# Kernel tuning notes

Hardware: AMD Instinct MI355X
Metric: run time of the kernel (lower is better)

The kernel has to match this reference:

```python
import jax, jax.numpy as jnp
import numpy as np

B, S, DIM = 2, 2048, 2048
QH, KVH = 32, 8
HD = DIM // QH            # 64
KV_DIM = HD * KVH         # 512
MAX_LEN = 2048
SCALE = HD ** -0.5
NEG_INF = -1e30


def _rope_cache(seq_len, head_dim, max_len, theta=10000.0, factor=8.0):
    # faithful to generate_sin_cos_pos_emb (causal branch, offset=0),
    # cache built at max_len then sliced to seq_len by the caller
    idx = np.arange(0, head_dim, 2, dtype=np.float64) / head_dim
    inv_freq = 1.0 / theta ** idx
    if factor > 1.0:
        seq_eff = max(max_len, max_len)  # generate called with seq_len=max_length
        adj = (factor * seq_eff / max_len - (factor - 1.0)) ** (head_dim / (head_dim - 2.0))
        inv_freq = 1.0 / (theta * adj) ** idx
    pos = np.arange(0, max_len, dtype=np.float64)
    freqs = np.einsum('i,j->ij', pos, inv_freq)
    emb = np.concatenate([freqs, freqs], axis=-1)  # [max_len, head_dim]
    cos = jnp.asarray(np.cos(emb)[:seq_len], dtype=jnp.float32)
    sin = jnp.asarray(np.sin(emb)[:seq_len], dtype=jnp.float32)
    return cos, sin


def _rotate_half(x):
    x1, x2 = jnp.split(x, 2, axis=-1)
    return jnp.concatenate([-x2, x1], axis=-1)


def _apply_rope(x, cos, sin):
    # x: [B, H, S, D]; cos/sin: [S, D]
    return x * cos + _rotate_half(x) * sin


def setup_inputs() -> dict:
    key = jax.random.key(0)
    ks = jax.random.split(key, 11)
    s = 0.02
    return {
        'query': jax.random.normal(ks[0], (B, S, DIM), jnp.float32),
        'key':   jax.random.normal(ks[1], (B, S, DIM), jnp.float32),
        'value': jax.random.normal(ks[2], (B, S, DIM), jnp.float32),
        'w_q': jax.random.normal(ks[3], (DIM, DIM), jnp.float32) * s,
        'b_q': jnp.zeros((DIM,), jnp.float32),
        'w_k': jax.random.normal(ks[4], (DIM, KV_DIM), jnp.float32) * s,
        'b_k': jnp.zeros((KV_DIM,), jnp.float32),
        'w_v': jax.random.normal(ks[5], (DIM, KV_DIM), jnp.float32) * s,
        'b_v': jnp.zeros((KV_DIM,), jnp.float32),
        'w_o': jax.random.normal(ks[6], (DIM, DIM), jnp.float32) * s,
        'b_o': jnp.zeros((DIM,), jnp.float32),
    }


def reference(query, key, value, w_q, b_q, w_k, b_k, w_v, b_v, w_o, b_o):
    # projections (weights stored as [in, out])
    q = query @ w_q + b_q                                    # [B,S,DIM]
    k = key   @ w_k + b_k                                    # [B,S,KV_DIM]
    v = value @ w_v + b_v                                    # [B,S,KV_DIM]

    q = q.reshape(B, S, QH, HD).transpose(0, 2, 1, 3)        # [B,QH,S,HD]
    k = k.reshape(B, S, KVH, HD).transpose(0, 2, 1, 3)       # [B,KVH,S,HD]
    v = v.reshape(B, S, KVH, HD).transpose(0, 2, 1, 3)       # [B,KVH,S,HD]

    cos, sin = _rope_cache(S, HD, MAX_LEN)
    q = _apply_rope(q, cos, sin)
    k = _apply_rope(k, cos, sin)

    # GQA: group queries per kv head (equivalent to repeat_interleave on K/V)
    G = QH // KVH
    qg = q.reshape(B, KVH, G, S, HD)
    scores = jnp.einsum('bhgqd,bhkd->bhgqk', qg, k) * SCALE  # [B,KVH,G,S,S]
    causal = jnp.tril(jnp.ones((S, S), dtype=bool))
    scores = jnp.where(causal, scores, NEG_INF)
    probs = jax.nn.softmax(scores, axis=-1)
    ctx = jnp.einsum('bhgqk,bhkd->bhgqd', probs, v)          # [B,KVH,G,S,HD]
    ctx = ctx.reshape(B, QH, S, HD).transpose(0, 2, 1, 3).reshape(B, S, DIM)
    return ctx @ w_o + b_o                                   # [B,S,DIM]
```

## Files before the change

kernel.cpp:

```cpp
#include <hip/hip_runtime.h>
#include <hip/hip_bf16.h>

typedef __hip_bfloat16 bf16_t;
typedef __attribute__((ext_vector_type(8))) short bf16x8;
typedef __attribute__((ext_vector_type(4))) float f32x4;

#define S_LEN   2048
#define D_MODEL 2048
#define N_QH    32
#define N_KVH   8
#define HEAD_D  64
#define KV_D    512
#define M_ROWS  4096
#define QK_SCALE (0.125f * 1.44269504088896340736f)
#define NQT     16

__global__ void wt_conv_all_kernel(const float* __restrict__ wq, const float* __restrict__ wk,
                                   const float* __restrict__ wv, const float* __restrict__ wo,
                                   bf16_t* __restrict__ tq, bf16_t* __restrict__ tk,
                                   bf16_t* __restrict__ tv, bf16_t* __restrict__ to,
                                   float* __restrict__ cosT, float* __restrict__ sinT) {
    const int x = blockIdx.x;
    if (x == 160) {
        int j = threadIdx.x & 31;
        double invf = pow(10000.0, -(double)(2 * j) / 64.0);
#pragma unroll
        for (int i = 0; i < 4; i++) {
            int pos = blockIdx.y * 32 + i * 8 + (threadIdx.x >> 5);
            double a = (double)pos * invf;
            cosT[pos * 32 + j] = (float)cos(a);
            sinT[pos * 32 + j] = (float)sin(a);
        }
        return;
    }
    __shared__ float tile[32][33];
    const float* W; bf16_t* Wt; int N, nb;
    if (x < 64)       { W = wq; Wt = tq; N = D_MODEL; nb = x; }
    else if (x < 80)  { W = wk; Wt = tk; N = KV_D;    nb = x - 64; }
    else if (x < 96)  { W = wv; Wt = tv; N = KV_D;    nb = x - 80; }
    else              { W = wo; Wt = to; N = D_MODEL; nb = x - 96; }
    const int K = D_MODEL;
    int n0 = nb * 32, k0 = blockIdx.y * 32;
    int tx = threadIdx.x & 31, ty = threadIdx.x >> 5;
#pragma unroll
    for (int i = 0; i < 4; i++) {
        int r = ty + i * 8;
        tile[r][tx] = W[(size_t)(k0 + r) * N + n0 + tx];
    }
    __syncthreads();
#pragma unroll
    for (int i = 0; i < 4; i++) {
        int r = ty + i * 8;
        Wt[(size_t)(n0 + r) * K + k0 + tx] = __float2bfloat16(tile[tx][r]);
    }
}

struct __align__(8) bf16x4s { bf16_t x, y, z, w; };

__device__ __forceinline__ void async_copy16(const bf16_t* g, bf16_t* l) {
    __builtin_amdgcn_global_load_lds((const __attribute__((address_space(1))) void*)g,
                                     (__attribute__((address_space(3))) void*)l, 16, 0, 0);
}

template <int ROPE, int OUTF32, int QSCALE>
__global__ __launch_bounds__(256, 2)
void gqa_gemm_kernel(const bf16_t* __restrict__ A, const bf16_t* __restrict__ Bt,
                     const float* __restrict__ bias, void* __restrict__ Cout,
                     int M, int N, int K,
                     const float* __restrict__ cosT, const float* __restrict__ sinT) {
    __shared__ __align__(16) bf16_t As[128 * 64];
    __shared__ __align__(16) bf16_t Bs[128 * 64];

    const int t = threadIdx.x;
    const int bx = blockIdx.x;
    const int xcd = bx & 7, j = bx >> 3;
    const int am0 = (((xcd >> 1) << 3) + (j >> 3)) * 128;
    const int bn0 = (((xcd & 1) << 3) + (j & 7)) * 128;

    const int l = t & 63, w = t >> 6;
    const int wr = w >> 1, wc = w & 1;
    const int lr = l & 15, lk = l >> 4;

    f32x4 acc[4][4];
#pragma unroll
    for (int i = 0; i < 4; i++)
#pragma unroll
        for (int jx = 0; jx < 4; jx++) acc[i][jx] = (f32x4)0.0f;

    const int r0 = t >> 3;
    const int c  = (t & 7) ^ (r0 & 7);
    const bf16_t* aptr = A + (size_t)(am0 + r0) * K + c * 8;
    const bf16_t* bptr = Bt + (size_t)(bn0 + r0) * K + c * 8;
    bf16_t* aLds = As + r0 * 64 + (t & 7) * 8;
    bf16_t* bLds = Bs + r0 * 64 + (t & 7) * 8;

    for (int k0 = 0; k0 < K; k0 += 64) {
#pragma unroll
        for (int s = 0; s < 4; ++s) {
            async_copy16(aptr + (size_t)(s * 32) * K + k0, aLds + s * 2048);
            async_copy16(bptr + (size_t)(s * 32) * K + k0, bLds + s * 2048);
        }
        __syncthreads();

        bf16x8 af[4][2], bfr[4][2];
#pragma unroll
        for (int mi = 0; mi < 4; mi++)
#pragma unroll
            for (int ks = 0; ks < 2; ks++)
                af[mi][ks] = *(const bf16x8*)&As[(wr * 64 + mi * 16 + lr) * 64 +
                                 ((ks * 32 + lk * 8) ^ ((lr & 7) << 3))];
#pragma unroll
        for (int ni = 0; ni < 4; ni++)
#pragma unroll
            for (int ks = 0; ks < 2; ks++)
                bfr[ni][ks] = *(const bf16x8*)&Bs[(wc * 64 + ni * 16 + lr) * 64 +
                                  ((ks * 32 + lk * 8) ^ ((lr & 7) << 3))];
#pragma unroll
        for (int mi = 0; mi < 4; mi++)
#pragma unroll
            for (int ni = 0; ni < 4; ni++)
#pragma unroll
                for (int ks = 0; ks < 2; ks++)
                    acc[mi][ni] = __builtin_amdgcn_mfma_f32_16x16x32_bf16(
                        af[mi][ks], bfr[ni][ks], acc[mi][ni], 0, 0, 0);
        __syncthreads();
    }

#pragma unroll
    for (int mi = 0; mi < 4; mi++) {
#pragma unroll
        for (int reg = 0; reg < 4; reg++) {
            int row = am0 + wr * 64 + mi * 16 + lk * 4 + reg;
            if (OUTF32) {
                float* out = (float*)Cout;
#pragma unroll
                for (int ni = 0; ni < 4; ni++) {
                    int col = bn0 + wc * 64 + ni * 16 + lr;
                    out[(size_t)row * N + col] = acc[mi][ni][reg] + bias[col];
                }
            } else if (ROPE) {
                bf16_t* out = (bf16_t*)Cout;
                int pos = row & (S_LEN - 1);
#pragma unroll
                for (int np = 0; np < 2; np++) {
                    int jj = np * 16 + lr;
                    float cs = cosT[pos * 32 + jj];
                    float sn = sinT[pos * 32 + jj];
                    int col1 = bn0 + wc * 64 + np * 16 + lr;
                    float x1 = acc[mi][np][reg] + bias[col1];
                    float x2 = acc[mi][np + 2][reg] + bias[col1 + 32];
                    float o1 = x1 * cs - x2 * sn;
                    float o2 = x2 * cs + x1 * sn;
                    if (QSCALE) { o1 *= QK_SCALE; o2 *= QK_SCALE; }
                    out[(size_t)row * N + col1]      = __float2bfloat16(o1);
                    out[(size_t)row * N + col1 + 32] = __float2bfloat16(o2);
                }
            } else {
                bf16_t* out = (bf16_t*)Cout;
#pragma unroll
                for (int ni = 0; ni < 4; ni++) {
                    int col = bn0 + wc * 64 + ni * 16 + lr;
                    out[(size_t)row * N + col] =
                        __float2bfloat16(acc[mi][ni][reg] + bias[col]);
                }
            }
        }
    }
}

__global__ __launch_bounds__(256, 4)
void gqa_kvc_kernel(const float* __restrict__ Key, const float* __restrict__ Val,
                    const float* __restrict__ Query,
                    const bf16_t* __restrict__ Wtk, const bf16_t* __restrict__ Wtv,
                    const float* __restrict__ bk, const float* __restrict__ bv,
                    bf16_t* __restrict__ Kout, bf16_t* __restrict__ VtOut,
                    bf16_t* __restrict__ Qbf,
                    const float* __restrict__ cosT, const float* __restrict__ sinT) {
    __shared__ __align__(16) char smem[9216];
    bf16_t* As  = (bf16_t*)smem;
    bf16_t* Bs  = (bf16_t*)(smem + 4096);
    bf16_t* VtE = (bf16_t*)smem;

    const int bx = blockIdx.x;
    const int t = threadIdx.x;

    if (bx >= 1024) {
        int tid = (bx - 1024) * 256 + t;
        const int total = M_ROWS * D_MODEL / 4;
#pragma unroll 4
        for (int i = tid; i < total; i += 512 * 256) {
            float4 v = ((const float4*)Query)[i];
            bf16x4s o;
            o.x = __float2bfloat16(v.x);
            o.y = __float2bfloat16(v.y);
            o.z = __float2bfloat16(v.z);
            o.w = __float2bfloat16(v.w);
            ((bf16x4s*)Qbf)[i] = o;
        }
        return;
    }

    constexpr int K = D_MODEL;
    const int xcd = bx & 7;
    const int j   = bx >> 3;
    const int z   = xcd >> 2;
    const int am0 = (((xcd & 3) << 4) + (j >> 3)) * 64;
    const int bn0 = (j & 7) * 64;

    const float* A32  = z ? Val : Key;
    const bf16_t* Bt  = z ? Wtv : Wtk;
    const float* bias = z ? bv : bk;

    const int l = t & 63, w = t >> 6;
    const int lr = l & 15, lk = l >> 4;

    f32x4 acc[4];
#pragma unroll
    for (int jx = 0; jx < 4; jx++) acc[jx] = (f32x4)0.0f;

    const int sr = t >> 2;
    const int sc = (t & 3) * 8;
    const float*  aptr = A32 + (size_t)(am0 + sr) * K + sc;
    const bf16_t* bptr = Bt + (size_t)(bn0 + sr) * K + sc;
    bf16_t* aLds = As + sr * 32 + sc;
    bf16_t* bLds = Bs + t * 8;

    float4 pa0 = ((const float4*)aptr)[0];
    float4 pa1 = ((const float4*)aptr)[1];

    for (int it = 0; it < K / 32; ++it) {
        union { bf16x8 v; bf16_t e[8]; } u;
        u.e[0] = __float2bfloat16(pa0.x); u.e[1] = __float2bfloat16(pa0.y);
        u.e[2] = __float2bfloat16(pa0.z); u.e[3] = __float2bfloat16(pa0.w);
        u.e[4] = __float2bfloat16(pa1.x); u.e[5] = __float2bfloat16(pa1.y);
        u.e[6] = __float2bfloat16(pa1.z); u.e[7] = __float2bfloat16(pa1.w);
        *(bf16x8*)aLds = u.v;
        async_copy16(bptr + it * 32, bLds);
        __builtin_amdgcn_sched_barrier(0);
        if (it + 1 < K / 32) {
            const float* ap = aptr + (it + 1) * 32;
            pa0 = ((const float4*)ap)[0];
            pa1 = ((const float4*)ap)[1];
            __builtin_amdgcn_sched_barrier(0);
            asm volatile("s_waitcnt lgkmcnt(0) vmcnt(2)" ::: "memory");
        } else {
            asm volatile("s_waitcnt lgkmcnt(0) vmcnt(0)" ::: "memory");
        }
        __builtin_amdgcn_sched_barrier(0);
        __builtin_amdgcn_s_barrier();
        __builtin_amdgcn_sched_barrier(0);

        bf16x8 af = *(const bf16x8*)&As[(w * 16 + lr) * 32 + lk * 8];
        bf16x8 bfr[4];
#pragma unroll
        for (int ni = 0; ni < 4; ni++)
            bfr[ni] = *(const bf16x8*)&Bs[(ni * 16 + lr) * 32 + lk * 8];
#pragma unroll
        for (int ni = 0; ni < 4; ni++)
            acc[ni] = __builtin_amdgcn_mfma_f32_16x16x32_bf16(af, bfr[ni], acc[ni], 0, 0, 0);
        __builtin_amdgcn_sched_barrier(0);
        __builtin_amdgcn_s_barrier();
        __builtin_amdgcn_sched_barrier(0);
    }

    if (z == 0) {
#pragma unroll
        for (int reg = 0; reg < 4; reg++) {
            int row = am0 + w * 16 + lk * 4 + reg;
            int pos = row & (S_LEN - 1);
#pragma unroll
            for (int np = 0; np < 2; np++) {
                int jj = np * 16 + lr;
                float cs = cosT[pos * 32 + jj];
                float sn = sinT[pos * 32 + jj];
                int col1 = bn0 + np * 16 + lr;
                float x1 = acc[np][reg] + bias[col1];
                float x2 = acc[np + 2][reg] + bias[col1 + 32];
                Kout[(size_t)row * KV_D + col1]      = __float2bfloat16(x1 * cs - x2 * sn);
                Kout[(size_t)row * KV_D + col1 + 32] = __float2bfloat16(x2 * cs + x1 * sn);
            }
        }
    } else {
        __syncthreads();
#pragma unroll
        for (int ni = 0; ni < 4; ni++) {
            bf16x4s pk;
            pk.x = __float2bfloat16(acc[ni][0] + bias[bn0 + ni * 16 + lr]);
            pk.y = __float2bfloat16(acc[ni][1] + bias[bn0 + ni * 16 + lr]);
            pk.z = __float2bfloat16(acc[ni][2] + bias[bn0 + ni * 16 + lr]);
            pk.w = __float2bfloat16(acc[ni][3] + bias[bn0 + ni * 16 + lr]);
            *(bf16x4s*)&VtE[(ni * 16 + lr) * 72 + w * 16 + lk * 4] = pk;
        }
        __syncthreads();
        const int d = t & 63, w2 = t >> 6;
        const int bI = am0 >> 11;
        const int kvhI = bn0 >> 6;
        const int sl = (am0 & (S_LEN - 1)) + w2 * 16;
        bf16_t* dst = VtOut + ((size_t)(bI * N_KVH + kvhI) * HEAD_D + d) * S_LEN + sl;
        const bf16_t* src = &VtE[d * 72 + w2 * 16];
        *(bf16x8*)dst       = *(const bf16x8*)src;
        *(bf16x8*)(dst + 8) = *(const bf16x8*)(src + 8);
    }
}

__device__ __forceinline__ void stage_K8(const bf16_t* KB, bf16_t* dst, int kt, int t) {
    const int skey = t >> 3;
    const int c    = (t & 7) ^ (skey & 7);
    async_copy16(KB + (size_t)(kt * 64 + skey) * KV_D + c * 8, dst + t * 8);
}
__device__ __forceinline__ void stage_V8(const bf16_t* VTb, bf16_t* dst, int kt, int t) {
    const int sd = t >> 3;
    const int c  = (t & 7) ^ (sd & 7);
    async_copy16(VTb + (size_t)sd * S_LEN + kt * 64 + c * 8, dst + t * 8);
}

__global__ __launch_bounds__(512, 4)
void gqa_attn_kernel(const bf16_t* __restrict__ Q, const bf16_t* __restrict__ Kb,
                     const bf16_t* __restrict__ VT, bf16_t* __restrict__ Ctx) {
    __shared__ __align__(16) bf16_t Ks[2][64 * 64];
    __shared__ __align__(16) bf16_t Vs[2][64 * 64];
    __shared__ __align__(16) bf16_t Pw[8][16 * 72];

    const int t = threadIdx.x, l = t & 63, w = t >> 6;
    const int lr = l & 15, lk = l >> 4;

    const int flat = blockIdx.x;
    const int xcd = flat & 7, j0 = flat >> 3;
    const int combo  = xcd * 2 + (j0 >> 5);
    const int within = j0 & 31;
    const int b   = combo >> 3;
    const int kvh = combo & 7;
    const int h   = kvh * 4 + (within >> 3);
    const int p   = within & 7;

    bf16x8 vones;
#pragma unroll
    for (int i = 0; i < 8; i++) vones[i] = (short)0x3F80;

    const bf16_t* KB  = Kb + (size_t)b * S_LEN * KV_D + kvh * HEAD_D;
    const bf16_t* VTb = VT + ((size_t)(b * N_KVH + kvh) * HEAD_D) * S_LEN;

#pragma unroll
    for (int half = 0; half < 2; ++half) {
        const int qt  = half ? (NQT - 1 - p) : p;
        const int q0w = qt * 128 + w * 16;
        const int qg  = q0w + lr;

        bf16x8 qf[2];
        {
            const bf16_t* qrow = Q + ((size_t)(b * S_LEN + qg)) * D_MODEL + h * HEAD_D;
            qf[0] = *(const bf16x8*)(qrow + lk * 8);
            qf[1] = *(const bf16x8*)(qrow + 32 + lk * 8);
        }

        f32x4 oaccT[4];
        f32x4 oaccS = (f32x4)0.0f;
#pragma unroll
        for (int df = 0; df < 4; df++) oaccT[df] = (f32x4)0.0f;

        const int nkt = 2 * qt + 2;

        stage_K8(KB, Ks[0], 0, t);
        stage_V8(VTb, Vs[0], 0, t);
        __syncthreads();

        int cur = 0;
        for (int kt = 0; kt < nkt; ++kt) {
            const bool pre = (kt + 1 < nkt);
            if (pre) {
                stage_K8(KB, Ks[cur ^ 1], kt + 1, t);
                stage_V8(VTb, Vs[cur ^ 1], kt + 1, t);
            }

            if (kt * 64 <= q0w + 15) {
                const bool diag = (kt * 64 + 63 > q0w);

                f32x4 sfrT[4];
#pragma unroll
                for (int ni = 0; ni < 4; ni++) sfrT[ni] = (f32x4)0.0f;
                __builtin_amdgcn_s_setprio(1);
#pragma unroll
                for (int ni = 0; ni < 4; ni++)
#pragma unroll
                    for (int ks = 0; ks < 2; ks++) {
                        bf16x8 kf = *(const bf16x8*)&Ks[cur][(ni * 16 + lr) * 64 +
                                        ((ks * 32 + lk * 8) ^ ((lr & 7) << 3))];
                        sfrT[ni] = __builtin_amdgcn_mfma_f32_16x16x32_bf16(kf, qf[ks],
                                                                           sfrT[ni], 0, 0, 0);
                    }
                __builtin_amdgcn_s_setprio(0);

#pragma unroll
                for (int ni = 0; ni < 4; ni++) {
                    float sc0 = sfrT[ni][0], sc1 = sfrT[ni][1];
                    float sc2 = sfrT[ni][2], sc3 = sfrT[ni][3];
                    if (diag) {
                        int kbase = kt * 64 + ni * 16 + lk * 4;
                        if (kbase + 0 > qg) sc0 = -1e30f;
                        if (kbase + 1 > qg) sc1 = -1e30f;
                        if (kbase + 2 > qg) sc2 = -1e30f;
                        if (kbase + 3 > qg) sc3 = -1e30f;
                    }
                    bf16x4s pk;
                    pk.x = __float2bfloat16(exp2f(sc0));
                    pk.y = __float2bfloat16(exp2f(sc1));
                    pk.z = __float2bfloat16(exp2f(sc2));
                    pk.w = __float2bfloat16(exp2f(sc3));
                    *(bf16x4s*)&Pw[w][lr * 72 + ni * 16 + lk * 4] = pk;
                }

                __builtin_amdgcn_s_setprio(1);
#pragma unroll
                for (int ks = 0; ks < 2; ks++) {
                    bf16x8 pf = *(const bf16x8*)&Pw[w][lr * 72 + ks * 32 + lk * 8];
                    oaccS = __builtin_amdgcn_mfma_f32_16x16x32_bf16(vones, pf, oaccS, 0, 0, 0);
#pragma unroll
                    for (int df = 0; df < 4; df++) {
                        bf16x8 vf = *(const bf16x8*)&Vs[cur][(df * 16 + lr) * 64 +
                                        ((ks * 32 + lk * 8) ^ ((lr & 7) << 3))];
                        oaccT[df] = __builtin_amdgcn_mfma_f32_16x16x32_bf16(vf, pf,
                                            oaccT[df], 0, 0, 0);
                    }
                }
                __builtin_amdgcn_s_setprio(0);
            }

            __syncthreads();
            cur ^= 1;
        }

        {
            float inv = 1.0f / oaccS[0];
            bf16_t* crow = Ctx + ((size_t)(b * S_LEN + qg)) * D_MODEL + h * HEAD_D;
#pragma unroll
            for (int df = 0; df < 4; df++) {
                bf16x4s ov;
                ov.x = __float2bfloat16(oaccT[df][0] * inv);
                ov.y = __float2bfloat16(oaccT[df][1] * inv);
                ov.z = __float2bfloat16(oaccT[df][2] * inv);
                ov.w = __float2bfloat16(oaccT[df][3] * inv);
                *(bf16x4s*)(crow + df * 16 + lk * 4) = ov;
            }
        }
    }
}

extern "C" void kernel_launch(void* const* d_in, const int* in_sizes, int n_in,
                              void* d_out, int out_size, void* d_ws, size_t ws_size,
                              hipStream_t stream) {
    const float* query = (const float*)d_in[0];
    const float* key_  = (const float*)d_in[1];
    const float* value = (const float*)d_in[2];
    const float* w_q = (const float*)d_in[3];
    const float* b_q = (const float*)d_in[4];
    const float* w_k = (const float*)d_in[5];
    const float* b_k = (const float*)d_in[6];
    const float* w_v = (const float*)d_in[7];
    const float* b_v = (const float*)d_in[8];
    const float* w_o = (const float*)d_in[9];
    const float* b_o = (const float*)d_in[10];
    float* out = (float*)d_out;

    char* ws = (char*)d_ws;
    bf16_t* Abuf = (bf16_t*)(ws);
    bf16_t* qb   = (bf16_t*)(ws + (size_t)(16 << 20));
    bf16_t* kb   = (bf16_t*)(ws + (size_t)(32 << 20));
    bf16_t* vt   = (bf16_t*)(ws + (size_t)(36 << 20));
    bf16_t* wtq  = (bf16_t*)(ws + (size_t)(40 << 20));
    bf16_t* wtk  = (bf16_t*)(ws + (size_t)(48 << 20));
    bf16_t* wtv  = (bf16_t*)(ws + (size_t)(50 << 20));
    bf16_t* wto  = (bf16_t*)(ws + (size_t)(52 << 20));
    float* cosT  = (float*)(ws + (size_t)(60 << 20));
    float* sinT  = (float*)(ws + (size_t)(60 << 20) + (256 << 10));

    wt_conv_all_kernel<<<dim3(161, 64), 256, 0, stream>>>(w_q, w_k, w_v, w_o,
                                                          wtq, wtk, wtv, wto, cosT, sinT);

    gqa_kvc_kernel<<<1536, 256, 0, stream>>>(key_, value, query, wtk, wtv,
                                             b_k, b_v, kb, vt, Abuf, cosT, sinT);

    gqa_gemm_kernel<1, 0, 1><<<512, 256, 0, stream>>>(
        Abuf, wtq, b_q, qb, M_ROWS, D_MODEL, D_MODEL, cosT, sinT);

    gqa_attn_kernel<<<512, 512, 0, stream>>>(qb, kb, vt, Abuf);

    gqa_gemm_kernel<0, 1, 0><<<512, 256, 0, stream>>>(
        Abuf, wto, b_o, out, M_ROWS, D_MODEL, D_MODEL, cosT, sinT);
}
```

Baseline: 211.2 us.

## Fuse Q/K/V projections into one GEMM launch after a single bf16 prep pass

```diff
diff --git a/kernel.cpp b/kernel.cpp
--- a/kernel.cpp
+++ b/kernel.cpp
@@ -15,47 +15,70 @@
 #define QK_SCALE (0.125f * 1.44269504088896340736f)
 #define NQT     16
 
-__global__ void wt_conv_all_kernel(const float* __restrict__ wq, const float* __restrict__ wk,
-                                   const float* __restrict__ wv, const float* __restrict__ wo,
-                                   bf16_t* __restrict__ tq, bf16_t* __restrict__ tk,
-                                   bf16_t* __restrict__ tv, bf16_t* __restrict__ to,
-                                   float* __restrict__ cosT, float* __restrict__ sinT) {
-    const int x = blockIdx.x;
-    if (x == 160) {
-        int j = threadIdx.x & 31;
+struct __align__(8) bf16x4s { bf16_t x, y, z, w; };
+
+__global__ void prep_kernel(const float* __restrict__ wq, const float* __restrict__ wk,
+                            const float* __restrict__ wv, const float* __restrict__ wo,
+                            bf16_t* __restrict__ tq, bf16_t* __restrict__ tk,
+                            bf16_t* __restrict__ tv, bf16_t* __restrict__ to,
+                            const float* __restrict__ query, const float* __restrict__ key_,
+                            const float* __restrict__ value,
+                            bf16_t* __restrict__ qbf, bf16_t* __restrict__ kbf,
+                            bf16_t* __restrict__ vbf,
+                            float* __restrict__ cosT, float* __restrict__ sinT) {
+    const int bx = blockIdx.x, t = threadIdx.x;
+    if (bx < 10240) {
+        __shared__ float tile[32][33];
+        const float* W; bf16_t* Wt; int N, nb, kt;
+        if (bx < 4096)      { W = wq; Wt = tq; N = D_MODEL; nb = bx & 63;          kt = bx >> 6; }
+        else if (bx < 5120) { int i = bx - 4096; W = wk; Wt = tk; N = KV_D; nb = i & 15; kt = i >> 4; }
+        else if (bx < 6144) { int i = bx - 5120; W = wv; Wt = tv; N = KV_D; nb = i & 15; kt = i >> 4; }
+        else                { int i = bx - 6144; W = wo; Wt = to; N = D_MODEL; nb = i & 63; kt = i >> 6; }
+        const int K = D_MODEL;
+        int n0 = nb * 32, k0 = kt * 32;
+        int tx = t & 31, ty = t >> 5;
+#pragma unroll
+        for (int i = 0; i < 4; i++) {
+            int r = ty + i * 8;
+            tile[r][tx] = W[(size_t)(k0 + r) * N + n0 + tx];
+        }
+        __syncthreads();
+#pragma unroll
+        for (int i = 0; i < 4; i++) {
+            int r = ty + i * 8;
+            Wt[(size_t)(n0 + r) * K + k0 + tx] = __float2bfloat16(tile[tx][r]);
+        }
+        return;
+    }
+    if (bx < 10304) {
+        int blk = bx - 10240;
+        int j = t & 31;
         double invf = pow(10000.0, -(double)(2 * j) / 64.0);
 #pragma unroll
         for (int i = 0; i < 4; i++) {
-            int pos = blockIdx.y * 32 + i * 8 + (threadIdx.x >> 5);
+            int pos = blk * 32 + i * 8 + (t >> 5);
             double a = (double)pos * invf;
             cosT[pos * 32 + j] = (float)cos(a);
             sinT[pos * 32 + j] = (float)sin(a);
         }
         return;
     }
-    __shared__ float tile[32][33];
-    const float* W; bf16_t* Wt; int N, nb;
-    if (x < 64)       { W = wq; Wt = tq; N = D_MODEL; nb = x; }
-    else if (x < 80)  { W = wk; Wt = tk; N = KV_D;    nb = x - 64; }
-    else if (x < 96)  { W = wv; Wt = tv; N = KV_D;    nb = x - 80; }
-    else              { W = wo; Wt = to; N = D_MODEL; nb = x - 96; }
-    const int K = D_MODEL;
-    int n0 = nb * 32, k0 = blockIdx.y * 32;
-    int tx = threadIdx.x & 31, ty = threadIdx.x >> 5;
-#pragma unroll
-    for (int i = 0; i < 4; i++) {
-        int r = ty + i * 8;
-        tile[r][tx] = W[(size_t)(k0 + r) * N + n0 + tx];
-    }
-    __syncthreads();
-#pragma unroll
-    for (int i = 0; i < 4; i++) {
-        int r = ty + i * 8;
-        Wt[(size_t)(n0 + r) * K + k0 + tx] = __float2bfloat16(tile[tx][r]);
-    }
-}
-
-struct __align__(8) bf16x4s { bf16_t x, y, z, w; };
+    const int per = M_ROWS * D_MODEL / 4;
+    int tid = (bx - 10304) * 256 + t;
+    for (int i = tid; i < 3 * per; i += 1536 * 256) {
+        const float* src; bf16_t* dst; int off;
+        if (i < per)          { src = query; dst = qbf; off = i; }
+        else if (i < 2 * per) { src = key_;  dst = kbf; off = i - per; }
+        else                  { src = value; dst = vbf; off = i - 2 * per; }
+        float4 v = ((const float4*)src)[off];
+        bf16x4s o;
+        o.x = __float2bfloat16(v.x);
+        o.y = __float2bfloat16(v.y);
+        o.z = __float2bfloat16(v.z);
+        o.w = __float2bfloat16(v.w);
+        ((bf16x4s*)dst)[off] = o;
+    }
+}
 
 __device__ __forceinline__ void async_copy16(const bf16_t* g, bf16_t* l) {
     __builtin_amdgcn_global_load_lds((const __attribute__((address_space(1))) void*)g,
@@ -168,139 +191,137 @@
     }
 }
 
-__global__ __launch_bounds__(256, 4)
-void gqa_kvc_kernel(const float* __restrict__ Key, const float* __restrict__ Val,
-                    const float* __restrict__ Query,
-                    const bf16_t* __restrict__ Wtk, const bf16_t* __restrict__ Wtv,
-                    const float* __restrict__ bk, const float* __restrict__ bv,
-                    bf16_t* __restrict__ Kout, bf16_t* __restrict__ VtOut,
-                    bf16_t* __restrict__ Qbf,
+__global__ __launch_bounds__(256, 2)
+void gqa_qkv_kernel(const bf16_t* __restrict__ Qbf, const bf16_t* __restrict__ Kbf,
+                    const bf16_t* __restrict__ Vbf,
+                    const bf16_t* __restrict__ Wtq, const bf16_t* __restrict__ Wtk,
+                    const bf16_t* __restrict__ Wtv,
+                    const float* __restrict__ bq, const float* __restrict__ bk,
+                    const float* __restrict__ bv,
+                    bf16_t* __restrict__ Qout, bf16_t* __restrict__ Kout,
+                    bf16_t* __restrict__ VtOut,
                     const float* __restrict__ cosT, const float* __restrict__ sinT) {
-    __shared__ __align__(16) char smem[9216];
-    bf16_t* As  = (bf16_t*)smem;
-    bf16_t* Bs  = (bf16_t*)(smem + 4096);
-    bf16_t* VtE = (bf16_t*)smem;
-
-    const int bx = blockIdx.x;
-    const int t = threadIdx.x;
-
-    if (bx >= 1024) {
-        int tid = (bx - 1024) * 256 + t;
-        const int total = M_ROWS * D_MODEL / 4;
-#pragma unroll 4
-        for (int i = tid; i < total; i += 512 * 256) {
-            float4 v = ((const float4*)Query)[i];
-            bf16x4s o;
-            o.x = __float2bfloat16(v.x);
-            o.y = __float2bfloat16(v.y);
-            o.z = __float2bfloat16(v.z);
-            o.w = __float2bfloat16(v.w);
-            ((bf16x4s*)Qbf)[i] = o;
-        }
+    __shared__ __align__(16) char smem[128 * 140 * 2];
+    bf16_t* As = (bf16_t*)smem;
+    bf16_t* Bs = (bf16_t*)(smem + 16384);
+    bf16_t* TT = (bf16_t*)smem;
+
+    const int t = threadIdx.x, bx = blockIdx.x;
+    constexpr int K = D_MODEL;
+
+    int am0, bn0, mode;
+    const bf16_t *A, *Bt; const float* bias;
+    if (bx < 512) {
+        int xcd = bx & 7, j = bx >> 3;
+        am0 = (((xcd >> 1) << 3) + (j >> 3)) * 128;
+        bn0 = (((xcd & 1) << 3) + (j & 7)) * 128;
+        A = Qbf; Bt = Wtq; bias = bq; mode = 0;
+    } else {
+        int idx = bx - 512;
+        int z = idx >> 7;
+        int xcd = idx & 7, jj = (idx & 127) >> 3;
+        am0 = (xcd * 4 + (jj & 3)) * 128;
+        bn0 = (jj >> 2) * 128;
+        A = z ? Vbf : Kbf; Bt = z ? Wtv : Wtk; bias = z ? bv : bk; mode = z ? 2 : 1;
+    }
+
+    const int l = t & 63, w = t >> 6;
+    const int wr = w >> 1, wc = w & 1;
+    const int lr = l & 15, lk = l >> 4;
+
+    f32x4 acc[4][4];
+#pragma unroll
+    for (int i = 0; i < 4; i++)
+#pragma unroll
+        for (int jx = 0; jx < 4; jx++) acc[i][jx] = (f32x4)0.0f;
+
+    const int r0 = t >> 3;
+    const int c  = (t & 7) ^ (r0 & 7);
+    const bf16_t* aptr = A + (size_t)(am0 + r0) * K + c * 8;
+    const bf16_t* bptr = Bt + (size_t)(bn0 + r0) * K + c * 8;
+    bf16_t* aLds = As + r0 * 64 + (t & 7) * 8;
+    bf16_t* bLds = Bs + r0 * 64 + (t & 7) * 8;
+
+    for (int k0 = 0; k0 < K; k0 += 64) {
+#pragma unroll
+        for (int s = 0; s < 4; ++s) {
+            async_copy16(aptr + (size_t)(s * 32) * K + k0, aLds + s * 2048);
+            async_copy16(bptr + (size_t)(s * 32) * K + k0, bLds + s * 2048);
+        }
+        __syncthreads();
+
+        bf16x8 af[4][2], bfr[4][2];
+#pragma unroll
+        for (int mi = 0; mi < 4; mi++)
+#pragma unroll
+            for (int ks = 0; ks < 2; ks++)
+                af[mi][ks] = *(const bf16x8*)&As[(wr * 64 + mi * 16 + lr) * 64 +
+                                 ((ks * 32 + lk * 8) ^ ((lr & 7) << 3))];
+#pragma unroll
+        for (int ni = 0; ni < 4; ni++)
+#pragma unroll
+            for (int ks = 0; ks < 2; ks++)
+                bfr[ni][ks] = *(const bf16x8*)&Bs[(wc * 64 + ni * 16 + lr) * 64 +
+                                  ((ks * 32 + lk * 8) ^ ((lr & 7) << 3))];
+#pragma unroll
+        for (int mi = 0; mi < 4; mi++)
+#pragma unroll
+            for (int ni = 0; ni < 4; ni++)
+#pragma unroll
+                for (int ks = 0; ks < 2; ks++)
+                    acc[mi][ni] = __builtin_amdgcn_mfma_f32_16x16x32_bf16(
+                        af[mi][ks], bfr[ni][ks], acc[mi][ni], 0, 0, 0);
+        __syncthreads();
+    }
+
+    if (mode == 2) {
+#pragma unroll
+        for (int mi = 0; mi < 4; mi++)
+#pragma unroll
+            for (int ni = 0; ni < 4; ni++) {
+                int colL = wc * 64 + ni * 16 + lr;
+                float bz = bias[bn0 + colL];
+                bf16x4s pk;
+                pk.x = __float2bfloat16(acc[mi][ni][0] + bz);
+                pk.y = __float2bfloat16(acc[mi][ni][1] + bz);
+                pk.z = __float2bfloat16(acc[mi][ni][2] + bz);
+                pk.w = __float2bfloat16(acc[mi][ni][3] + bz);
+                *(bf16x4s*)&TT[colL * 140 + wr * 64 + mi * 16 + lk * 4] = pk;
+            }
+        __syncthreads();
+        const int colL = t >> 1, s0 = (t & 1) * 64;
+        const int cg = bn0 + colL;
+        const int bI = am0 >> 11;
+        bf16_t* dst = VtOut + ((size_t)(bI * N_KVH + (cg >> 6)) * HEAD_D + (cg & 63)) * S_LEN
+                      + (am0 & (S_LEN - 1)) + s0;
+        const bf16_t* src = &TT[colL * 140 + s0];
+#pragma unroll
+        for (int i = 0; i < 8; i++)
+            *(bf16x8*)(dst + i * 8) = *(const bf16x8*)(src + i * 8);
         return;
     }
 
-    constexpr int K = D_MODEL;
-    const int xcd = bx & 7;
-    const int j   = bx >> 3;
-    const int z   = xcd >> 2;
-    const int am0 = (((xcd & 3) << 4) + (j >> 3)) * 64;
-    const int bn0 = (j & 7) * 64;
-
-    const float* A32  = z ? Val : Key;
-    const bf16_t* Bt  = z ? Wtv : Wtk;
-    const float* bias = z ? bv : bk;
-
-    const int l = t & 63, w = t >> 6;
-    const int lr = l & 15, lk = l >> 4;
-
-    f32x4 acc[4];
-#pragma unroll
-    for (int jx = 0; jx < 4; jx++) acc[jx] = (f32x4)0.0f;
-
-    const int sr = t >> 2;
-    const int sc = (t & 3) * 8;
-    const float*  aptr = A32 + (size_t)(am0 + sr) * K + sc;
-    const bf16_t* bptr = Bt + (size_t)(bn0 + sr) * K + sc;
-    bf16_t* aLds = As + sr * 32 + sc;
-    bf16_t* bLds = Bs + t * 8;
-
-    float4 pa0 = ((const float4*)aptr)[0];
-    float4 pa1 = ((const float4*)aptr)[1];
-
-    for (int it = 0; it < K / 32; ++it) {
-        union { bf16x8 v; bf16_t e[8]; } u;
-        u.e[0] = __float2bfloat16(pa0.x); u.e[1] = __float2bfloat16(pa0.y);
-        u.e[2] = __float2bfloat16(pa0.z); u.e[3] = __float2bfloat16(pa0.w);
-        u.e[4] = __float2bfloat16(pa1.x); u.e[5] = __float2bfloat16(pa1.y);
-        u.e[6] = __float2bfloat16(pa1.z); u.e[7] = __float2bfloat16(pa1.w);
-        *(bf16x8*)aLds = u.v;
-        async_copy16(bptr + it * 32, bLds);
-        __builtin_amdgcn_sched_barrier(0);
-        if (it + 1 < K / 32) {
-            const float* ap = aptr + (it + 1) * 32;
-            pa0 = ((const float4*)ap)[0];
-            pa1 = ((const float4*)ap)[1];
-            __builtin_amdgcn_sched_barrier(0);
-            asm volatile("s_waitcnt lgkmcnt(0) vmcnt(2)" ::: "memory");
-        } else {
-            asm volatile("s_waitcnt lgkmcnt(0) vmcnt(0)" ::: "memory");
-        }
-        __builtin_amdgcn_sched_barrier(0);
-        __builtin_amdgcn_s_barrier();
-        __builtin_amdgcn_sched_barrier(0);
-
-        bf16x8 af = *(const bf16x8*)&As[(w * 16 + lr) * 32 + lk * 8];
-        bf16x8 bfr[4];
-#pragma unroll
-        for (int ni = 0; ni < 4; ni++)
-            bfr[ni] = *(const bf16x8*)&Bs[(ni * 16 + lr) * 32 + lk * 8];
-#pragma unroll
-        for (int ni = 0; ni < 4; ni++)
-            acc[ni] = __builtin_amdgcn_mfma_f32_16x16x32_bf16(af, bfr[ni], acc[ni], 0, 0, 0);
-        __builtin_amdgcn_sched_barrier(0);
-        __builtin_amdgcn_s_barrier();
-        __builtin_amdgcn_sched_barrier(0);
-    }
-
-    if (z == 0) {
+    const int N = (mode == 0) ? D_MODEL : KV_D;
+    bf16_t* out = (mode == 0) ? Qout : Kout;
+    const float qs = (mode == 0) ? QK_SCALE : 1.0f;
+#pragma unroll
+    for (int mi = 0; mi < 4; mi++)
 #pragma unroll
         for (int reg = 0; reg < 4; reg++) {
-            int row = am0 + w * 16 + lk * 4 + reg;
+            int row = am0 + wr * 64 + mi * 16 + lk * 4 + reg;
             int pos = row & (S_LEN - 1);
 #pragma unroll
             for (int np = 0; np < 2; np++) {
                 int jj = np * 16 + lr;
                 float cs = cosT[pos * 32 + jj];
                 float sn = sinT[pos * 32 + jj];
-                int col1 = bn0 + np * 16 + lr;
-                float x1 = acc[np][reg] + bias[col1];
-                float x2 = acc[np + 2][reg] + bias[col1 + 32];
-                Kout[(size_t)row * KV_D + col1]      = __float2bfloat16(x1 * cs - x2 * sn);
-                Kout[(size_t)row * KV_D + col1 + 32] = __float2bfloat16(x2 * cs + x1 * sn);
+                int col1 = bn0 + wc * 64 + np * 16 + lr;
+                float x1 = acc[mi][np][reg] + bias[col1];
+                float x2 = acc[mi][np + 2][reg] + bias[col1 + 32];
+                out[(size_t)row * N + col1]      = __float2bfloat16((x1 * cs - x2 * sn) * qs);
+                out[(size_t)row * N + col1 + 32] = __float2bfloat16((x2 * cs + x1 * sn) * qs);
             }
         }
-    } else {
-        __syncthreads();
-#pragma unroll
-        for (int ni = 0; ni < 4; ni++) {
-            bf16x4s pk;
-            pk.x = __float2bfloat16(acc[ni][0] + bias[bn0 + ni * 16 + lr]);
-            pk.y = __float2bfloat16(acc[ni][1] + bias[bn0 + ni * 16 + lr]);
-            pk.z = __float2bfloat16(acc[ni][2] + bias[bn0 + ni * 16 + lr]);
-            pk.w = __float2bfloat16(acc[ni][3] + bias[bn0 + ni * 16 + lr]);
-            *(bf16x4s*)&VtE[(ni * 16 + lr) * 72 + w * 16 + lk * 4] = pk;
-        }
-        __syncthreads();
-        const int d = t & 63, w2 = t >> 6;
-        const int bI = am0 >> 11;
-        const int kvhI = bn0 >> 6;
-        const int sl = (am0 & (S_LEN - 1)) + w2 * 16;
-        bf16_t* dst = VtOut + ((size_t)(bI * N_KVH + kvhI) * HEAD_D + d) * S_LEN + sl;
-        const bf16_t* src = &VtE[d * 72 + w2 * 16];
-        *(bf16x8*)dst       = *(const bf16x8*)src;
-        *(bf16x8*)(dst + 8) = *(const bf16x8*)(src + 8);
-    }
 }
 
 __device__ __forceinline__ void stage_K8(const bf16_t* KB, bf16_t* dst, int kt, int t) {
@@ -462,7 +483,7 @@
     float* out = (float*)d_out;
 
     char* ws = (char*)d_ws;
-    bf16_t* Abuf = (bf16_t*)(ws);
+    bf16_t* qbf  = (bf16_t*)(ws);
     bf16_t* qb   = (bf16_t*)(ws + (size_t)(16 << 20));
     bf16_t* kb   = (bf16_t*)(ws + (size_t)(32 << 20));
     bf16_t* vt   = (bf16_t*)(ws + (size_t)(36 << 20));
@@ -472,18 +493,17 @@
     bf16_t* wto  = (bf16_t*)(ws + (size_t)(52 << 20));
     float* cosT  = (float*)(ws + (size_t)(60 << 20));
     float* sinT  = (float*)(ws + (size_t)(60 << 20) + (256 << 10));
-
-    wt_conv_all_kernel<<<dim3(161, 64), 256, 0, stream>>>(w_q, w_k, w_v, w_o,
-                                                          wtq, wtk, wtv, wto, cosT, sinT);
-
-    gqa_kvc_kernel<<<1536, 256, 0, stream>>>(key_, value, query, wtk, wtv,
-                                             b_k, b_v, kb, vt, Abuf, cosT, sinT);
-
-    gqa_gemm_kernel<1, 0, 1><<<512, 256, 0, stream>>>(
-        Abuf, wtq, b_q, qb, M_ROWS, D_MODEL, D_MODEL, cosT, sinT);
-
-    gqa_attn_kernel<<<512, 512, 0, stream>>>(qb, kb, vt, Abuf);
+    bf16_t* kbf  = (bf16_t*)(ws + (size_t)(61 << 20));
+    bf16_t* vbf  = (bf16_t*)(ws + (size_t)(77 << 20));
+
+    prep_kernel<<<11840, 256, 0, stream>>>(w_q, w_k, w_v, w_o, wtq, wtk, wtv, wto,
+                                           query, key_, value, qbf, kbf, vbf, cosT, sinT);
+
+    gqa_qkv_kernel<<<768, 256, 0, stream>>>(qbf, kbf, vbf, wtq, wtk, wtv,
+                                            b_q, b_k, b_v, qb, kb, vt, cosT, sinT);
+
+    gqa_attn_kernel<<<512, 512, 0, stream>>>(qb, kb, vt, qbf);
 
     gqa_gemm_kernel<0, 1, 0><<<512, 256, 0, stream>>>(
-        Abuf, wto, b_o, out, M_ROWS, D_MODEL, D_MODEL, cosT, sinT);
-}
+        qbf, wto, b_o, out, M_ROWS, D_MODEL, D_MODEL, cosT, sinT);
+}
```

New measurement: 203.5 us. 1.04x faster.
